# Performance work log

Measured on AMD Instinct MI355X. Metric: run time of the kernel, lower is better.

Reference implementation:

```python
import jax, jax.numpy as jnp
import numpy as np

PC = (-60.0, -60.0, -4.0, 140.0, 60.0, 4.0)
BEV_H, BEV_W, E, HEADS, LVLS, PTS, ZN, CAMS = 50, 50, 256, 8, 3, 4, 4, 6
HD = E // HEADS
IMG_H, IMG_W = 512.0, 800.0
SHAPES = ((64, 100), (32, 50), (16, 25))
FFN = 2 * E
EPS = 1e-5


def grid_sample(img, grid):
    # img (B,C,H,W), grid (B,Hg,Wg,2) in [-1,1]; bilinear, zeros padding, align_corners=False
    B, C, H, W = img.shape
    Hg, Wg = grid.shape[1], grid.shape[2]
    x = (grid[..., 0] + 1.0) * (W * 0.5) - 0.5
    y = (grid[..., 1] + 1.0) * (H * 0.5) - 0.5
    x0 = jnp.floor(x)
    y0 = jnp.floor(y)
    wx = x - x0
    wy = y - y0
    x0i = x0.astype(jnp.int32)
    y0i = y0.astype(jnp.int32)
    imgf = img.reshape(B, C, H * W)

    def gather(ix, iy):
        valid = ((ix >= 0) & (ix < W) & (iy >= 0) & (iy < H)).astype(img.dtype)
        idx = jnp.clip(iy, 0, H - 1) * W + jnp.clip(ix, 0, W - 1)
        idx = jnp.broadcast_to(idx.reshape(B, 1, Hg * Wg), (B, C, Hg * Wg))
        return jnp.take_along_axis(imgf, idx, axis=2).reshape(B, C, Hg, Wg) * valid[:, None]

    v00 = gather(x0i, y0i)
    v01 = gather(x0i + 1, y0i)
    v10 = gather(x0i, y0i + 1)
    v11 = gather(x0i + 1, y0i + 1)
    wx = wx[:, None]
    wy = wy[:, None]
    return v00 * (1 - wy) * (1 - wx) + v01 * (1 - wy) * wx + v10 * wy * (1 - wx) + v11 * wy * wx


def layer_norm(x, g, b):
    m = x.mean(-1, keepdims=True)
    v = ((x - m) ** 2).mean(-1, keepdims=True)
    return (x - m) / jnp.sqrt(v + 1e-5) * g + b


def get_reference_points():
    xs = (jnp.arange(BEV_W, dtype=jnp.float32) + 0.5) / BEV_W
    ys = (jnp.arange(BEV_H, dtype=jnp.float32) + 0.5) / BEV_H
    zs = (jnp.arange(ZN, dtype=jnp.float32) + 0.5) / ZN
    ref_y, ref_x = jnp.meshgrid(ys, xs, indexing='ij')
    xy = jnp.stack([ref_x, ref_y], -1).reshape(-1, 2)  # (HW,2)
    xy = jnp.broadcast_to(xy[:, None, :], (BEV_H * BEV_W, ZN, 2))
    z = jnp.broadcast_to(zs[None, :, None], (BEV_H * BEV_W, ZN, 1))
    r = jnp.concatenate([xy, z], -1)  # (HW,Z,3), normalized
    scale = jnp.array([PC[3] - PC[0], PC[4] - PC[1], PC[5] - PC[2]], jnp.float32)
    off = jnp.array([PC[0], PC[1], PC[2]], jnp.float32)
    return (r * scale + off).reshape(-1, 3)  # (HW*Z, 3)


def point_sampling(ref3d, l2i):
    # ref3d (Nq,3), l2i (B,N,4,4) -> ref2d (B,N,Nq,2), mask (B,N,Nq)
    Nq = ref3d.shape[0]
    pts = jnp.concatenate([ref3d, jnp.ones((Nq, 1), ref3d.dtype)], -1)
    cam = jnp.einsum('bnij,qj->bnqi', l2i, pts)
    d = cam[..., 2]
    u = cam[..., 0] / (d + EPS) / IMG_W
    v = cam[..., 1] / (d + EPS) / IMG_H
    ref2d = jnp.stack([u, v], -1)
    mask = (d > EPS) & (u > 0.0) & (u < 1.0) & (v > 0.0) & (v < 1.0)
    return ref2d, mask


def mha(q, k, v, fl):
    B = q.shape[0]
    wq, wk, wv = jnp.split(fl['ta_in_w'], 3, 0)
    bq, bk, bv = jnp.split(fl['ta_in_b'], 3, 0)
    Q = (q @ wq.T + bq).reshape(B, -1, HEADS, HD)
    K = (k @ wk.T + bk).reshape(B, -1, HEADS, HD)
    V = (v @ wv.T + bv).reshape(B, -1, HEADS, HD)
    a = jax.nn.softmax(jnp.einsum('bqhd,bkhd->bhqk', Q, K) / np.float32(np.sqrt(HD)), -1)
    o = jnp.einsum('bhqk,bkhd->bqhd', a, V).reshape(B, -1, E)
    return o @ fl['ta_out_w'].T + fl['ta_out_b']


def msda(query, qpos, value, ref, fl):
    # MultiScaleDeformableAttention (identity = zeros). ref (B,Nq,L,2) in [0,1].
    B, Nq, _ = query.shape
    q = query + qpos
    v = (value @ fl['vp_w'].T + fl['vp_b']).reshape(B, -1, HEADS, HD)
    off = (q @ fl['so_w'].T + fl['so_b']).reshape(B, Nq, HEADS, LVLS, PTS, 2)
    aw = jax.nn.softmax((q @ fl['aw_w'].T + fl['aw_b']).reshape(B, Nq, HEADS, LVLS * PTS), -1)
    aw = aw.reshape(B, Nq, HEADS, LVLS, PTS)
    norm = jnp.array([[w, h] for (h, w) in SHAPES], jnp.float32)  # (L,2) = (W,H)
    loc = ref[:, :, None, :, None, :] + off / norm[None, None, None, :, None, :]
    outs = []
    start = 0
    for l, (Hl, Wl) in enumerate(SHAPES):
        vl = v[:, start:start + Hl * Wl].transpose(0, 2, 3, 1).reshape(B * HEADS, HD, Hl, Wl)
        g = (2.0 * loc[:, :, :, l] - 1.0).transpose(0, 2, 1, 3, 4).reshape(B * HEADS, Nq, PTS, 2)
        outs.append(grid_sample(vl, g))  # (B*HEADS, HD, Nq, PTS)
        start += Hl * Wl
    s = jnp.stack(outs, 3)  # (B*HEADS, HD, Nq, L, P)
    w = aw.transpose(0, 2, 1, 3, 4).reshape(B * HEADS, 1, Nq, LVLS, PTS)
    o = (s * w).sum((3, 4)).reshape(B, HEADS, HD, Nq).transpose(0, 3, 1, 2).reshape(B, Nq, E)
    return o @ fl['op_w'].T + fl['op_b']


def spatial_attn(query, qpos, feats_t, l2i, ref3d, fl):
    B, Nq, _ = query.shape
    ref2d, mask = point_sampling(ref3d, l2i)
    out = jnp.zeros_like(query)
    valid = jnp.zeros((B, Nq), query.dtype)
    for cam in range(CAMS):
        value = jnp.concatenate(
            [f[:, cam].reshape(B, E, -1).transpose(0, 2, 1) for f in feats_t], axis=1)
        ref = jnp.broadcast_to(ref2d[:, cam][:, :, None, :], (B, Nq, LVLS, 2))
        a = msda(query, qpos, value, ref, fl)
        wgt = mask[:, cam].astype(query.dtype)
        out = out + a * wgt[..., None]
        valid = valid + wgt
    return out / jnp.maximum(valid, 1.0)[..., None]


def temporal_align(prev_bev, motion):
    B, C, H, W = prev_bev.shape
    xs = jnp.arange(W, dtype=prev_bev.dtype)
    ys = jnp.arange(H, dtype=prev_bev.dtype)
    yy, xx = jnp.meshgrid(ys, xs, indexing='ij')
    rx = (xx + 0.5) / W * (PC[3] - PC[0]) + PC[0]
    ry = (yy + 0.5) / H * (PC[4] - PC[1]) + PC[1]
    g = jnp.stack([rx, ry, jnp.zeros_like(rx), jnp.ones_like(rx)], -1)  # (H,W,4)
    inv = jnp.linalg.inv(motion)  # (B,4,4)
    gp = jnp.einsum('bij,hwj->bhwi', inv, g)
    nx = (gp[..., 0] - PC[0]) / (PC[3] - PC[0]) * 2.0 - 1.0
    ny = (gp[..., 1] - PC[1]) / (PC[4] - PC[1]) * 2.0 - 1.0
    return grid_sample(prev_bev, jnp.stack([nx, ny], -1))


def layer_fwd(bev, bev_pos, prev, feats_t, l2i, ref3d, fl):
    if prev is not None:
        attn = mha(bev + bev_pos, prev + bev_pos, prev, fl)
        bev = layer_norm(bev + attn, fl['n1_g'], fl['n1_b'])
    B, Nq, C = bev.shape
    bev_z = jnp.broadcast_to(bev[:, :, None, :], (B, Nq, ZN, C)).reshape(B, -1, C)
    pos_z = jnp.broadcast_to(bev_pos[:, :, None, :], (B, Nq, ZN, C)).reshape(B, -1, C)
    so = spatial_attn(bev_z, pos_z, feats_t, l2i, ref3d, fl)
    so = so.reshape(B, Nq, ZN, C).mean(2)
    bev = layer_norm(bev + so, fl['n2_g'], fl['n2_b'])
    h = jax.nn.relu(bev @ fl['ffn_w1'].T + fl['ffn_b1'])
    ffn = h @ fl['ffn_w2'].T + fl['ffn_b2']
    return layer_norm(bev + ffn, fl['n3_g'], fl['n3_b'])


def forward(fl, batch_size, seq_len):
    feats = [fl['feat0'], fl['feat1'], fl['feat2']]
    feats = [f.reshape(batch_size, seq_len, CAMS, E, f.shape[-2], f.shape[-1]) for f in feats]
    bev = jnp.broadcast_to(fl['bev_emb'][None], (batch_size, BEV_H * BEV_W, E))
    bev_pos = jnp.broadcast_to(fl['bev_pos_emb'][None], (batch_size, BEV_H * BEV_W, E))
    ref3d = get_reference_points()
    prev = None
    for t in range(seq_len):
        feats_t = [f[:, t] for f in feats]
        prev_al = None
        if prev is not None:
            pa = temporal_align(prev, fl['ego_motion'][:, t])
            prev_al = pa.reshape(batch_size, E, -1).transpose(0, 2, 1)
        bev_t = layer_fwd(bev, bev_pos, prev_al, feats_t, fl['lidar2img'][:, t], ref3d, fl)
        prev = bev_t.transpose(0, 2, 1).reshape(batch_size, E, BEV_H, BEV_W)
    return prev


def _make_cam_matrices():
    mats = np.zeros((CAMS, 4, 4), np.float32)
    K = np.array([[500.0, 0.0, 400.0], [0.0, 500.0, 256.0], [0.0, 0.0, 1.0]], np.float32)
    for i in range(CAMS):
        th = 2.0 * np.pi * i / CAMS
        xr = np.array([-np.sin(th), np.cos(th), 0.0])
        yr = np.array([0.0, 0.0, -1.0])
        fr = np.array([np.cos(th), np.sin(th), 0.0])
        R = np.stack([xr, yr, fr]).astype(np.float32)
        mats[i, :3, :3] = K @ R
        mats[i, 3, 3] = 1.0
    return mats


def setup_inputs() -> dict:
    key = jax.random.key(0)
    ks = jax.random.split(key, 20)
    rn = lambda k, s, sc=0.02: jax.random.normal(k, s, jnp.float32) * sc
    NOFF = HEADS * LVLS * PTS * 2
    NAW = HEADS * LVLS * PTS
    d = {
        'bev_emb': rn(ks[0], (BEV_H * BEV_W, E), 1.0),
        'bev_pos_emb': rn(ks[1], (BEV_H * BEV_W, E), 1.0),
        'ta_in_w': rn(ks[2], (3 * E, E)), 'ta_in_b': jnp.zeros(3 * E, jnp.float32),
        'ta_out_w': rn(ks[3], (E, E)), 'ta_out_b': jnp.zeros(E, jnp.float32),
        'so_w': rn(ks[4], (NOFF, E)), 'so_b': rn(ks[5], (NOFF,), 0.5),
        'aw_w': rn(ks[6], (NAW, E)), 'aw_b': jnp.zeros(NAW, jnp.float32),
        'vp_w': rn(ks[7], (E, E)), 'vp_b': jnp.zeros(E, jnp.float32),
        'op_w': rn(ks[8], (E, E)), 'op_b': jnp.zeros(E, jnp.float32),
        'ffn_w1': rn(ks[9], (FFN, E)), 'ffn_b1': jnp.zeros(FFN, jnp.float32),
        'ffn_w2': rn(ks[10], (E, FFN)), 'ffn_b2': jnp.zeros(E, jnp.float32),
        'n1_g': jnp.ones(E, jnp.float32), 'n1_b': jnp.zeros(E, jnp.float32),
        'n2_g': jnp.ones(E, jnp.float32), 'n2_b': jnp.zeros(E, jnp.float32),
        'n3_g': jnp.ones(E, jnp.float32), 'n3_b': jnp.zeros(E, jnp.float32),
        'feat0': rn(ks[11], (12, E, 64, 100), 1.0),
        'feat1': rn(ks[12], (12, E, 32, 50), 1.0),
        'feat2': rn(ks[13], (12, E, 16, 25), 1.0),
    }
    mats = _make_cam_matrices()  # realistic lidar->img projections per camera
    d['lidar2img'] = jnp.asarray(np.broadcast_to(mats, (1, 2, CAMS, 4, 4)).copy())
    em = np.tile(np.eye(4, dtype=np.float32), (1, 2, 1, 1))
    em[..., 0, 3] = 2.0  # 2m forward ego translation per step
    d['ego_motion'] = jnp.asarray(em)
    d['batch_size'] = 1
    d['seq_len'] = 2
    return d


def reference(bev_emb, bev_pos_emb, ta_in_w, ta_in_b, ta_out_w, ta_out_b,
              so_w, so_b, aw_w, aw_b, vp_w, vp_b, op_w, op_b,
              ffn_w1, ffn_b1, ffn_w2, ffn_b2,
              n1_g, n1_b, n2_g, n2_b, n3_g, n3_b,
              feat0, feat1, feat2, lidar2img, ego_motion, batch_size, seq_len):
    fl = dict(bev_emb=bev_emb, bev_pos_emb=bev_pos_emb, ta_in_w=ta_in_w, ta_in_b=ta_in_b,
              ta_out_w=ta_out_w, ta_out_b=ta_out_b, so_w=so_w, so_b=so_b, aw_w=aw_w, aw_b=aw_b,
              vp_w=vp_w, vp_b=vp_b, op_w=op_w, op_b=op_b, ffn_w1=ffn_w1, ffn_b1=ffn_b1,
              ffn_w2=ffn_w2, ffn_b2=ffn_b2, n1_g=n1_g, n1_b=n1_b, n2_g=n2_g, n2_b=n2_b,
              n3_g=n3_g, n3_b=n3_b, feat0=feat0, feat1=feat1, feat2=feat2,
              lidar2img=lidar2img, ego_motion=ego_motion)
    return forward(fl, int(batch_size), int(seq_len))
```

## Files before the change

### kernel.cpp

```cpp
#include <hip/hip_runtime.h>
#include <hip/hip_bf16.h>

#define NPIX   2500
#define EDIM   256
#define NHEADS 8
#define HDIM   32
#define NLVLS  3
#define NPTS   4
#define NZ     4
#define NCAMS  6
#define NQTOT  10000
#define NVAL   8400
#define FFND   512
#define NCHUNK 10
#define KVCH   250
#define VTROW  2504

typedef __attribute__((ext_vector_type(8))) short short8;
typedef __attribute__((ext_vector_type(4))) float float4v;

__device__ __forceinline__ void level_params(int l, int& H, int& W, int& st) {
    if (l == 0)      { H = 64; W = 100; st = 0;    }
    else if (l == 1) { H = 32; W = 50;  st = 6400; }
    else             { H = 16; W = 25;  st = 8000; }
}

__device__ __forceinline__ unsigned short f2bf(float x) {
    unsigned int u = __builtin_bit_cast(unsigned int, x);
    return (unsigned short)((u + 0x7fffu + ((u >> 16) & 1u)) >> 16);
}

__global__ __launch_bounds__(256) void transpose_feat_all_k(const float* __restrict__ feat0,
                                                            const float* __restrict__ feat1,
                                                            const float* __restrict__ feat2,
                                                            int t,
                                                            unsigned short* __restrict__ featT)
{
    const int cam = blockIdx.z;
    const int bx = blockIdx.x;
    const float* feat; int HW, lvl_off, p0;
    if (bx < 200)      { feat = feat0; HW = 6400; lvl_off = 0;    p0 = bx * 32;         }
    else if (bx < 250) { feat = feat1; HW = 1600; lvl_off = 6400; p0 = (bx - 200) * 32; }
    else               { feat = feat2; HW = 400;  lvl_off = 8000; p0 = (bx - 250) * 32; }
    const float* F = feat + (size_t)(t * NCAMS + cam) * EDIM * HW;
    unsigned short* T = featT + (size_t)cam * NVAL * EDIM;
    __shared__ float tile[32][33];
    const int e0 = blockIdx.y * 32;
    const int tp = threadIdx.x & 31, tr = threadIdx.x >> 5;
#pragma unroll
    for (int i = 0; i < 4; i++) {
        int e = e0 + tr + i * 8;
        int p = p0 + tp;
        tile[tr + i * 8][tp] = (p < HW) ? F[(size_t)e * HW + p] : 0.f;
    }
    __syncthreads();
#pragma unroll
    for (int i = 0; i < 4; i++) {
        int p = p0 + tr + i * 8;
        int e = e0 + tp;
        if (p < HW) T[(size_t)(lvl_off + p) * EDIM + e] = f2bf(tile[tp][tr + i * 8]);
    }
}

template<int ACT, int ADD>
__global__ __launch_bounds__(256) void gemm64_k(const float* __restrict__ A,
                                                const float* __restrict__ A2,
                                                const float* __restrict__ W,
                                                const float* __restrict__ bias,
                                                float* __restrict__ C,
                                                int M, int N, int K,
                                                size_t a_bs, size_t w_bs,
                                                size_t b_bs, size_t c_bs)
{
    __shared__ unsigned short As[64][44];
    __shared__ unsigned short Ws[64][44];
    const int m0 = blockIdx.y * 64;
    const int n0 = blockIdx.x * 64;
    const int tid = threadIdx.x;
    const float* Af = A + blockIdx.z * a_bs;
    const float* Wf = W + blockIdx.z * w_bs;
    const float* Bf = bias ? bias + blockIdx.z * b_bs : nullptr;
    float* Cb = C + blockIdx.z * c_bs;
    const int wave = tid >> 6, lane = tid & 63;
    const int wr = wave >> 1, wc = wave & 1;
    const int fr = lane & 15, fk = lane >> 4;
    float4v acc[2][2];
#pragma unroll
    for (int mi = 0; mi < 2; mi++)
#pragma unroll
        for (int ni = 0; ni < 2; ni++) { acc[mi][ni][0] = 0.f; acc[mi][ni][1] = 0.f;
                                         acc[mi][ni][2] = 0.f; acc[mi][ni][3] = 0.f; }
    const int srow = tid >> 2, sk = (tid & 3) * 8;
    for (int k0 = 0; k0 < K; k0 += 32) {
        unsigned short tmp[8];
        {
            const int gr = m0 + srow;
            if (gr < M) {
                const float* src = Af + (size_t)gr * K + k0 + sk;
                if (ADD) {
                    const float* src2 = A2 + (size_t)gr * K + k0 + sk;
#pragma unroll
                    for (int j = 0; j < 8; j++) tmp[j] = f2bf(src[j] + src2[j]);
                } else {
#pragma unroll
                    for (int j = 0; j < 8; j++) tmp[j] = f2bf(src[j]);
                }
            } else {
#pragma unroll
                for (int j = 0; j < 8; j++) tmp[j] = 0;
            }
            *(short8*)&As[srow][sk] = *(short8*)&tmp[0];
        }
        {
            const int gw = n0 + srow;
            if (gw < N) {
                const float* src = Wf + (size_t)gw * K + k0 + sk;
#pragma unroll
                for (int j = 0; j < 8; j++) tmp[j] = f2bf(src[j]);
            } else {
#pragma unroll
                for (int j = 0; j < 8; j++) tmp[j] = 0;
            }
            *(short8*)&Ws[srow][sk] = *(short8*)&tmp[0];
        }
        __syncthreads();
        short8 af[2], bfr[2];
#pragma unroll
        for (int mi = 0; mi < 2; mi++)
            af[mi] = *(const short8*)&As[wr * 32 + mi * 16 + fr][fk * 8];
#pragma unroll
        for (int ni = 0; ni < 2; ni++)
            bfr[ni] = *(const short8*)&Ws[wc * 32 + ni * 16 + fr][fk * 8];
#pragma unroll
        for (int mi = 0; mi < 2; mi++)
#pragma unroll
            for (int ni = 0; ni < 2; ni++)
                acc[mi][ni] = __builtin_amdgcn_mfma_f32_16x16x32_bf16(
                    af[mi], bfr[ni], acc[mi][ni], 0, 0, 0);
        __syncthreads();
    }
#pragma unroll
    for (int mi = 0; mi < 2; mi++)
#pragma unroll
        for (int ni = 0; ni < 2; ni++) {
            const int col = n0 + wc * 32 + ni * 16 + fr;
#pragma unroll
            for (int r = 0; r < 4; r++) {
                const int row = m0 + wr * 32 + mi * 16 + fk * 4 + r;
                if (row < M && col < N) {
                    float v = acc[mi][ni][r] + (Bf ? Bf[col] : 0.f);
                    if (ACT) v = fmaxf(v, 0.f);
                    Cb[(size_t)row * N + col] = v;
                }
            }
        }
}

template<int ACT, int ADD>
__global__ __launch_bounds__(256) void gemm64o_k(const float* __restrict__ A,
                                                 const float* __restrict__ A2,
                                                 const float* __restrict__ W,
                                                 const float* __restrict__ bias,
                                                 unsigned short* __restrict__ C,
                                                 int M, int N, int K)
{
    __shared__ unsigned short As[64][44];
    __shared__ unsigned short Ws[64][44];
    const int m0 = blockIdx.y * 64;
    const int n0 = blockIdx.x * 64;
    const int tid = threadIdx.x;
    const int wave = tid >> 6, lane = tid & 63;
    const int wr = wave >> 1, wc = wave & 1;
    const int fr = lane & 15, fk = lane >> 4;
    float4v acc[2][2];
#pragma unroll
    for (int mi = 0; mi < 2; mi++)
#pragma unroll
        for (int ni = 0; ni < 2; ni++) { acc[mi][ni][0] = 0.f; acc[mi][ni][1] = 0.f;
                                         acc[mi][ni][2] = 0.f; acc[mi][ni][3] = 0.f; }
    const int srow = tid >> 2, sk = (tid & 3) * 8;
    for (int k0 = 0; k0 < K; k0 += 32) {
        unsigned short tmp[8];
// ... 196 lines not shown
                for (int j = 0; j < 8; j++) tmp[j] = f2bf(src[j]);
            } else {
#pragma unroll
                for (int j = 0; j < 8; j++) tmp[j] = 0;
            }
            *(short8*)&Ws[srow][sk] = *(short8*)&tmp[0];
        }
        __syncthreads();
        short8 af[2], bfr[2];
#pragma unroll
        for (int mi = 0; mi < 2; mi++)
            af[mi] = *(const short8*)&As[wr * 32 + mi * 16 + fr][fk * 8];
#pragma unroll
        for (int ni = 0; ni < 2; ni++)
            bfr[ni] = *(const short8*)&Ws[wc * 32 + ni * 16 + fr][fk * 8];
#pragma unroll
        for (int mi = 0; mi < 2; mi++)
#pragma unroll
            for (int ni = 0; ni < 2; ni++)
                acc[mi][ni] = __builtin_amdgcn_mfma_f32_16x16x32_bf16(
                    af[mi], bfr[ni], acc[mi][ni], 0, 0, 0);
        __syncthreads();
    }
#pragma unroll
    for (int mi = 0; mi < 2; mi++)
#pragma unroll
        for (int ni = 0; ni < 2; ni++) {
            const int col = n0 + wc * 32 + ni * 16 + fr;
#pragma unroll
            for (int r = 0; r < 4; r++) {
                const int row = m0 + wr * 32 + mi * 16 + fk * 4 + r;
                if (row < M && col < N)
                    Cb[(size_t)row * N + col] = acc[mi][ni][r] + (bias ? bias[col] : 0.f);
            }
        }
}

__global__ __launch_bounds__(256) void gemm_vs_k(const unsigned short* __restrict__ featT,
                                                 const float* __restrict__ vp_w,
                                                 const float* __restrict__ vp_b,
                                                 float* __restrict__ vproj,
                                                 const float* __restrict__ Aso,
                                                 const float* __restrict__ A2so,
                                                 const float* __restrict__ Wso,
                                                 const float* __restrict__ Waw,
                                                 const float* __restrict__ Bso,
                                                 const float* __restrict__ Baw,
                                                 float* __restrict__ Cso)
{
    const int z = blockIdx.z;
    const bool so = (z == 6);
    if (!so && blockIdx.x >= 4) return;
    if (so && blockIdx.y >= 40) return;
    __shared__ unsigned short As[64][44];
    __shared__ unsigned short Ws[64][44];
    const int m0 = blockIdx.y * 64;
    const int n0 = blockIdx.x * 64;
    const int tid = threadIdx.x;
    const int wave = tid >> 6, lane = tid & 63;
    const int wr = wave >> 1, wc = wave & 1;
    const int fr = lane & 15, fk = lane >> 4;
    const unsigned short* Af = featT + (size_t)z * NVAL * EDIM;
    const int M = so ? NPIX : NVAL;
    float4v acc[2][2];
#pragma unroll
    for (int mi = 0; mi < 2; mi++)
#pragma unroll
        for (int ni = 0; ni < 2; ni++) { acc[mi][ni][0] = 0.f; acc[mi][ni][1] = 0.f;
                                         acc[mi][ni][2] = 0.f; acc[mi][ni][3] = 0.f; }
    const int srow = tid >> 2, sk = (tid & 3) * 8;
    for (int k0 = 0; k0 < EDIM; k0 += 32) {
        unsigned short tmp[8];
        {
            const int gr = m0 + srow;
            if (so) {
                if (gr < NPIX) {
                    const float* src  = Aso  + (size_t)gr * EDIM + k0 + sk;
                    const float* src2 = A2so + (size_t)gr * EDIM + k0 + sk;
#pragma unroll
                    for (int j = 0; j < 8; j++) tmp[j] = f2bf(src[j] + src2[j]);
                } else {
#pragma unroll
                    for (int j = 0; j < 8; j++) tmp[j] = 0;
                }
                *(short8*)&As[srow][sk] = *(short8*)&tmp[0];
            } else {
                if (gr < NVAL) {
                    *(short8*)&As[srow][sk] =
                        *(const short8*)&Af[(size_t)gr * EDIM + k0 + sk];
                } else {
                    short8 zr = {0,0,0,0,0,0,0,0};
                    *(short8*)&As[srow][sk] = zr;
                }
            }
        }
        {
            const int gw = n0 + srow;
            const float* src;
            if (so)
                src = (gw < 192) ? Wso + (size_t)gw * EDIM + k0 + sk
                    : (gw < 288) ? Waw + (size_t)(gw - 192) * EDIM + k0 + sk
                                 : nullptr;
            else
                src = vp_w + (size_t)gw * EDIM + k0 + sk;
            if (src) {
#pragma unroll
                for (int j = 0; j < 8; j++) tmp[j] = f2bf(src[j]);
            } else {
#pragma unroll
                for (int j = 0; j < 8; j++) tmp[j] = 0;
            }
            *(short8*)&Ws[srow][sk] = *(short8*)&tmp[0];
        }
        __syncthreads();
        short8 af[2], bfr[2];
#pragma unroll
        for (int mi = 0; mi < 2; mi++)
            af[mi] = *(const short8*)&As[wr * 32 + mi * 16 + fr][fk * 8];
#pragma unroll
        for (int ni = 0; ni < 2; ni++)
            bfr[ni] = *(const short8*)&Ws[wc * 32 + ni * 16 + fr][fk * 8];
#pragma unroll
        for (int mi = 0; mi < 2; mi++)
#pragma unroll
            for (int ni = 0; ni < 2; ni++)
                acc[mi][ni] = __builtin_amdgcn_mfma_f32_16x16x32_bf16(
                    af[mi], bfr[ni], acc[mi][ni], 0, 0, 0);
        __syncthreads();
    }
#pragma unroll
    for (int mi = 0; mi < 2; mi++)
#pragma unroll
        for (int ni = 0; ni < 2; ni++) {
            const int col = n0 + wc * 32 + ni * 16 + fr;
#pragma unroll
            for (int r = 0; r < 4; r++) {
                const int row = m0 + wr * 32 + mi * 16 + fk * 4 + r;
                if (row < M) {
                    if (so) {
                        if (col < 288) {
                            const float b = (col < 192) ? Bso[col] : Baw[col - 192];
                            Cso[(size_t)row * 288 + col] = acc[mi][ni][r] + b;
                        }
                    } else {
                        vproj[((size_t)z * NVAL + row) * EDIM + col] =
                            acc[mi][ni][r] + vp_b[col];
                    }
                }
            }
        }
}

__global__ __launch_bounds__(256) void gemm_op_k(const float* __restrict__ S,
                                                 const float* __restrict__ validn,
                                                 const float* __restrict__ W,
                                                 float* __restrict__ C)
{
    __shared__ unsigned short As[64][44];
    __shared__ unsigned short Ws[64][44];
    __shared__ float sfac[256];
    const int m0 = blockIdx.y * 64;
    const int n0 = blockIdx.x * 64;
    const int tid = threadIdx.x;
    {
        const int idx = m0 * 4 + tid;
        const float vn = (idx < NQTOT) ? validn[idx] : 1.f;
        sfac[tid] = 1.f / fmaxf(vn, 1.f);
    }
    __syncthreads();
    const int wave = tid >> 6, lane = tid & 63;
    const int wr = wave >> 1, wc = wave & 1;
    const int fr = lane & 15, fk = lane >> 4;
    float4v acc[2][2];
#pragma unroll
    for (int mi = 0; mi < 2; mi++)
#pragma unroll
        for (int ni = 0; ni < 2; ni++) { acc[mi][ni][0] = 0.f; acc[mi][ni][1] = 0.f;
                                         acc[mi][ni][2] = 0.f; acc[mi][ni][3] = 0.f; }
    const int srow = tid >> 2, sk = (tid & 3) * 8;
    for (int k0 = 0; k0 < EDIM; k0 += 32) {
        unsigned short tmp[8];
        {
            const int gr = m0 + srow;
            if (gr < NPIX) {
                float sum[8];
#pragma unroll
                for (int j = 0; j < 8; j++) sum[j] = 0.f;
#pragma unroll
                for (int iz = 0; iz < NZ; iz++) {
                    const float* src = S + ((size_t)(gr * 4 + iz) * EDIM + k0 + sk);
                    const float f = sfac[srow * 4 + iz];
#pragma unroll
                    for (int j = 0; j < 8; j++) sum[j] += src[j] * f;
                }
#pragma unroll
                for (int j = 0; j < 8; j++) tmp[j] = f2bf(sum[j] * 0.25f);
            } else {
#pragma unroll
                for (int j = 0; j < 8; j++) tmp[j] = 0;
            }
            *(short8*)&As[srow][sk] = *(short8*)&tmp[0];
        }
        {
            const float* src = W + (size_t)(n0 + srow) * EDIM + k0 + sk;
#pragma unroll
            for (int j = 0; j < 8; j++) tmp[j] = f2bf(src[j]);
            *(short8*)&Ws[srow][sk] = *(short8*)&tmp[0];
        }
        __syncthreads();
        short8 af[2], bfr[2];
#pragma unroll
        for (int mi = 0; mi < 2; mi++)
            af[mi] = *(const short8*)&As[wr * 32 + mi * 16 + fr][fk * 8];
#pragma unroll
        for (int ni = 0; ni < 2; ni++)
            bfr[ni] = *(const short8*)&Ws[wc * 32 + ni * 16 + fr][fk * 8];
#pragma unroll
        for (int mi = 0; mi < 2; mi++)
#pragma unroll
            for (int ni = 0; ni < 2; ni++)
                acc[mi][ni] = __builtin_amdgcn_mfma_f32_16x16x32_bf16(
                    af[mi], bfr[ni], acc[mi][ni], 0, 0, 0);
        __syncthreads();
    }
#pragma unroll
    for (int mi = 0; mi < 2; mi++)
#pragma unroll
        for (int ni = 0; ni < 2; ni++) {
            const int col = n0 + wc * 32 + ni * 16 + fr;
#pragma unroll
            for (int r = 0; r < 4; r++) {
                const int row = m0 + wr * 32 + mi * 16 + fk * 4 + r;
                if (row < NPIX)
                    C[(size_t)row * EDIM + col] = acc[mi][ni][r];
            }
        }
}

template<int TRANS>
__global__ __launch_bounds__(256) void resid_ln_k(const float* __restrict__ x0,
                                                  const float* __restrict__ x1,
                                                  const float* __restrict__ cvec,
                                                  const float* __restrict__ cscale,
                                                  const float* __restrict__ g,
                                                  const float* __restrict__ bta,
                                                  float* __restrict__ out)
{
    const int row = blockIdx.x, e = threadIdx.x;
    float x = x0[(size_t)row * EDIM + e] + x1[(size_t)row * EDIM + e];
    if (cvec) x += cvec[e] * cscale[row];
    __shared__ float red[256];
    red[e] = x; __syncthreads();
    for (int s = 128; s > 0; s >>= 1) { if (e < s) red[e] += red[e + s]; __syncthreads(); }
    float mean = red[0] * (1.f / 256.f);
    __syncthreads();
    float dx = x - mean;
    red[e] = dx * dx; __syncthreads();
    for (int s = 128; s > 0; s >>= 1) { if (e < s) red[e] += red[e + s]; __syncthreads(); }
    float var = red[0] * (1.f / 256.f);
    const float res = dx * rsqrtf(var + 1e-5f) * g[e] + bta[e];
    if (TRANS)
        out[(size_t)e * NPIX + row] = res;
    else
        out[(size_t)row * EDIM + e] = res;
}

__global__ void uv_aw_k(const float* __restrict__ l2i, int t,
                        const float* __restrict__ raw,
                        float* __restrict__ uvtab,
                        float* __restrict__ validn,
                        float* __restrict__ aw_soft,
                        float* __restrict__ vbm)
{
    if (blockIdx.x < 40) {
        const int n = blockIdx.x * 256 + threadIdx.x;
        if (n >= NQTOT) return;
        const int pix = n >> 2, iz = n & 3;
        const int prow = pix / 50, pcol = pix % 50;
        const float x3 = (pcol + 0.5f) * 4.0f - 60.f;
        const float y3 = (prow + 0.5f) * 2.4f - 60.f;
        const float z3 = (iz + 0.5f) * 2.0f - 4.f;
        int vcount = 0;
        float buf[12];
#pragma unroll
        for (int cam = 0; cam < NCAMS; cam++) {
            const float* Mt = l2i + (size_t)(t * NCAMS + cam) * 16;
            const float p0 = Mt[0] * x3 + Mt[1] * y3 + Mt[2]  * z3 + Mt[3];
            const float p1 = Mt[4] * x3 + Mt[5] * y3 + Mt[6]  * z3 + Mt[7];
            const float p2 = Mt[8] * x3 + Mt[9] * y3 + Mt[10] * z3 + Mt[11];
            const float dd = p2 + 1e-5f;
            const float u = p0 / dd * (1.f / 800.f);
            const float v = p1 / dd * (1.f / 512.f);
            const bool valid = (p2 > 1e-5f) && (u > 0.f) && (u < 1.f) &&
                               (v > 0.f) && (v < 1.f);
            if (valid) vcount++;
            buf[cam * 2]     = valid ? u : -1.f;
            buf[cam * 2 + 1] = v;
        }
#pragma unroll
        for (int j = 0; j < 12; j++) uvtab[(size_t)n * 12 + j] = buf[j];
        validn[n] = (float)vcount;
        float ind = (vcount > 0) ? 1.f : 0.f;
        ind += __shfl_xor(ind, 1);
        ind += __shfl_xor(ind, 2);
        if (iz == 0) vbm[pix] = ind * 0.25f;
    } else {
        const int gidx = (blockIdx.x - 40) * 256 + threadIdx.x;
        if (gidx >= NPIX * NHEADS) return;
        const int pix = gidx / NHEADS, h = gidx % NHEADS;
        const float* p = raw + (size_t)pix * 288 + 192 + h * 12;
        float m = -3.0e38f;
#pragma unroll
        for (int j = 0; j < 12; j++) m = fmaxf(m, p[j]);
        float e[12]; float s = 0.f;
#pragma unroll
        for (int j = 0; j < 12; j++) { e[j] = __expf(p[j] - m); s += e[j]; }
        const float inv = 1.f / s;
        float* o = aw_soft + (size_t)pix * 96 + h * 12;
#pragma unroll
        for (int j = 0; j < 12; j++) o[j] = e[j] * inv;
    }
}

__global__ __launch_bounds__(256) void spatial_sample_k(const float* __restrict__ vproj,
                                                        const float* __restrict__ offb,
                                                        const float* __restrict__ awb,
                                                        const float* __restrict__ uvtab,
                                                        float* __restrict__ S)
{
    const int n = blockIdx.x;
    const int tid = threadIdx.x;
    const int wave = tid >> 6, lane = tid & 63;
    const int ch0 = lane << 2;
    const int h = lane >> 3;
    const int pix = n >> 2;
    __shared__ float soff[192];
    __shared__ float saw[96];
    __shared__ float suv[12];
    __shared__ float red[3][256];
    if (tid < 192) soff[tid] = offb[(size_t)pix * 288 + tid];
    if (tid < 96)  saw[tid]  = awb[(size_t)pix * 96 + tid];
    if (tid >= 192 && tid < 204) suv[tid - 192] = uvtab[(size_t)n * 12 + (tid - 192)];
    __syncthreads();
    float4 acc = make_float4(0.f, 0.f, 0.f, 0.f);
    for (int cam = 0; cam < NCAMS; cam++) {
        const float u = suv[cam * 2];
        if (u < 0.f) continue;
        const float v = suv[cam * 2 + 1];
        const float* vc = vproj + (size_t)cam * NVAL * EDIM + ch0;
        for (int pt = wave; pt < NLVLS * NPTS; pt += 4) {
            const int l = pt >> 2, p = pt & 3;
            int Hl, Wl, st; level_params(l, Hl, Wl, st);
            const int ob = ((h * NLVLS + l) * NPTS + p) * 2;
            const float x = u * (float)Wl + soff[ob]     - 0.5f;
            const float y = v * (float)Hl + soff[ob + 1] - 0.5f;
            const float xf = floorf(x), yf = floorf(y);
            const float wx = x - xf, wy = y - yf;
            const int x0 = (int)xf, y0 = (int)yf;
            const float a = saw[(h * NLVLS + l) * NPTS + p];
            const bool xi0 = (x0 >= 0) & (x0 < Wl);
            const bool xi1 = (x0 + 1 >= 0) & (x0 + 1 < Wl);
            const bool yi0 = (y0 >= 0) & (y0 < Hl);
            const bool yi1 = (y0 + 1 >= 0) & (y0 + 1 < Hl);
            const int rb = st + y0 * Wl + x0;
            float4 sv = make_float4(0.f, 0.f, 0.f, 0.f);
            if (yi0 & xi0) {
                const float w00 = (1.f - wy) * (1.f - wx);
                const float4 t4 = *(const float4*)(vc + ((size_t)rb << 8));
                sv.x += w00 * t4.x; sv.y += w00 * t4.y; sv.z += w00 * t4.z; sv.w += w00 * t4.w;
            }
            if (yi0 & xi1) {
                const float w01 = (1.f - wy) * wx;
                const float4 t4 = *(const float4*)(vc + ((size_t)(rb + 1) << 8));
                sv.x += w01 * t4.x; sv.y += w01 * t4.y; sv.z += w01 * t4.z; sv.w += w01 * t4.w;
            }
            if (yi1 & xi0) {
                const float w10 = wy * (1.f - wx);
                const float4 t4 = *(const float4*)(vc + ((size_t)(rb + Wl) << 8));
                sv.x += w10 * t4.x; sv.y += w10 * t4.y; sv.z += w10 * t4.z; sv.w += w10 * t4.w;
            }
            if (yi1 & xi1) {
                const float w11 = wy * wx;
                const float4 t4 = *(const float4*)(vc + ((size_t)(rb + Wl + 1) << 8));
                sv.x += w11 * t4.x; sv.y += w11 * t4.y; sv.z += w11 * t4.z; sv.w += w11 * t4.w;
            }
            acc.x += a * sv.x; acc.y += a * sv.y; acc.z += a * sv.z; acc.w += a * sv.w;
        }
    }
    if (wave > 0) *(float4*)&red[wave - 1][ch0] = acc;
    __syncthreads();
    if (wave == 0) {
#pragma unroll
        for (int w2 = 0; w2 < 3; w2++) {
            const float4 r4 = *(const float4*)&red[w2][ch0];
            acc.x += r4.x; acc.y += r4.y; acc.z += r4.z; acc.w += r4.w;
        }
        *(float4*)(S + (size_t)n * EDIM + ch0) = acc;
    }
}

__global__ __launch_bounds__(256) void talign_k(const float* __restrict__ prev,
                                                const float* __restrict__ motion,
                                                float* __restrict__ out)
{
    __shared__ float sinv[16];
    if (threadIdx.x == 0) {
        float a[4][8];
        for (int i = 0; i < 4; i++)
            for (int j = 0; j < 4; j++) { a[i][j] = motion[i * 4 + j];
                                          a[i][4 + j] = (i == j) ? 1.f : 0.f; }
        for (int col = 0; col < 4; col++) {
            int piv = col;
            for (int r = col + 1; r < 4; r++)
                if (fabsf(a[r][col]) > fabsf(a[piv][col])) piv = r;
            if (piv != col)
                for (int j = 0; j < 8; j++) { float tp = a[col][j];
                                              a[col][j] = a[piv][j]; a[piv][j] = tp; }
            float idv = 1.f / a[col][col];
            for (int j = 0; j < 8; j++) a[col][j] *= idv;
            for (int r = 0; r < 4; r++) {
                if (r == col) continue;
                float f = a[r][col];
                for (int j = 0; j < 8; j++) a[r][j] -= f * a[col][j];
            }
        }
        for (int i = 0; i < 4; i++)
            for (int j = 0; j < 4; j++) sinv[i * 4 + j] = a[i][4 + j];
    }
    __syncthreads();
    const int pix = blockIdx.x, e = threadIdx.x;
    const int r = pix / 50, c = pix % 50;
    const float rx = (c + 0.5f) * 4.0f - 60.f;
    const float ry = (r + 0.5f) * 2.4f - 60.f;
    const float gx = sinv[0] * rx + sinv[1] * ry + sinv[3];
    const float gy = sinv[4] * rx + sinv[5] * ry + sinv[7];
    const float nx = (gx + 60.f) * 0.01f - 1.f;
    const float ny = (gy + 60.f) * (1.f / 60.f) - 1.f;
    const float x = (nx + 1.f) * 25.f - 0.5f;
    const float y = (ny + 1.f) * 25.f - 0.5f;
    const float xf = floorf(x), yf = floorf(y);
    const float wx = x - xf, wy = y - yf;
    const int x0 = (int)xf, y0 = (int)yf;
    bool xi0 = (x0 >= 0 && x0 < 50), xi1 = (x0 + 1 >= 0 && x0 + 1 < 50);
    bool yi0 = (y0 >= 0 && y0 < 50), yi1 = (y0 + 1 >= 0 && y0 + 1 < 50);
    float s = 0.f;
    if (yi0 && xi0) s += (1.f - wy) * (1.f - wx) * prev[(size_t)(y0 * 50 + x0) * EDIM + e];
    if (yi0 && xi1) s += (1.f - wy) * wx         * prev[(size_t)(y0 * 50 + x0 + 1) * EDIM + e];
    if (yi1 && xi0) s += wy * (1.f - wx)         * prev[(size_t)((y0 + 1) * 50 + x0) * EDIM + e];
    if (yi1 && xi1) s += wy * wx                 * prev[(size_t)((y0 + 1) * 50 + x0 + 1) * EDIM + e];
    out[(size_t)pix * EDIM + e] = s;
}

__global__ __launch_bounds__(256) void mha_mfma_k(const unsigned short* __restrict__ Qbf,
                                                  const unsigned short* __restrict__ Kbf,
                                                  const unsigned short* __restrict__ VbfT,
                                                  float* __restrict__ pacc,
                                                  float* __restrict__ pml)
{
    const int h = blockIdx.y;
    const int q0 = blockIdx.x * 64;
    const int chunk = blockIdx.z;
    const int kv0 = chunk * KVCH;
    const int kv1 = min(NPIX, kv0 + KVCH);
    const int tid = threadIdx.x;
    const int wave = tid >> 6, lane = tid & 63;
    const int fr = lane & 15, fk = lane >> 4;

    __shared__ unsigned short Qs[64][44];
    __shared__ unsigned short Ks[64][44];
    __shared__ unsigned short Vt[32][76];
    __shared__ unsigned short Ps[4][16][76];

    const int srow = tid >> 2, scs = tid & 3;
    {
        const int gq = q0 + srow;
        if (gq < NPIX)
            *(short8*)&Qs[srow][scs * 8] =
                *(const short8*)&Qbf[(size_t)gq * EDIM + h * HDIM + scs * 8];
        else {
            short8 z = {0,0,0,0,0,0,0,0};
            *(short8*)&Qs[srow][scs * 8] = z;
        }
    }
    __syncthreads();
    const short8 aq = *(const short8*)&Qs[wave * 16 + fr][fk * 8];

    float m[4], l[4];
    float4v o0, o1;
#pragma unroll
    for (int r = 0; r < 4; r++) { m[r] = -3.0e38f; l[r] = 0.f; o0[r] = 0.f; o1[r] = 0.f; }

    const int vd = tid >> 3, vpart = tid & 7;
    for (int kb = kv0; kb < kv1; kb += 64) {
        __syncthreads();
        {
// ... 8 lines not shown
            const unsigned short* vrow = VbfT + (size_t)(h * HDIM + vd) * VTROW;
            const int base = kb + vpart * 8;
            if (base + 8 <= kv1) {
                *(short8*)&Vt[vd][vpart * 8] = *(const short8*)&vrow[base];
            } else {
#pragma unroll
                for (int j = 0; j < 8; j++)
                    Vt[vd][vpart * 8 + j] = (base + j < kv1) ? vrow[base + j] : 0;
            }
        }
        __syncthreads();
        float4v s[4];
#pragma unroll
        for (int t = 0; t < 4; t++) {
            const short8 bk = *(const short8*)&Ks[t * 16 + fr][fk * 8];
            float4v z; z[0] = 0.f; z[1] = 0.f; z[2] = 0.f; z[3] = 0.f;
            s[t] = __builtin_amdgcn_mfma_f32_16x16x32_bf16(aq, bk, z, 0, 0, 0);
        }
        if (kb + 64 > kv1) {
#pragma unroll
            for (int t = 0; t < 4; t++) {
                const int colg = kb + t * 16 + fr;
                if (colg >= kv1) { s[t][0] = -3.0e38f; s[t][1] = -3.0e38f;
                                   s[t][2] = -3.0e38f; s[t][3] = -3.0e38f; }
            }
        }
        float cand[4];
#pragma unroll
        for (int r = 0; r < 4; r++)
            cand[r] = fmaxf(fmaxf(s[0][r], s[1][r]), fmaxf(s[2][r], s[3][r]));
#pragma unroll
        for (int off = 1; off < 16; off <<= 1)
#pragma unroll
            for (int r = 0; r < 4; r++)
                cand[r] = fmaxf(cand[r], __shfl_xor(cand[r], off));
        float corr[4];
#pragma unroll
        for (int r = 0; r < 4; r++) {
            const float mn = fmaxf(m[r], cand[r]);
            corr[r] = __expf(m[r] - mn);
            m[r] = mn;
        }
        float psum[4];
#pragma unroll
        for (int r = 0; r < 4; r++) psum[r] = 0.f;
#pragma unroll
        for (int t = 0; t < 4; t++)
#pragma unroll
            for (int r = 0; r < 4; r++) {
                const float p = __expf(s[t][r] - m[r]);
                psum[r] += p;
                Ps[wave][fk * 4 + r][t * 16 + fr] = f2bf(p);
            }
#pragma unroll
        for (int off = 1; off < 16; off <<= 1)
#pragma unroll
            for (int r = 0; r < 4; r++)
                psum[r] += __shfl_xor(psum[r], off);
#pragma unroll
        for (int r = 0; r < 4; r++) {
            l[r] = l[r] * corr[r] + psum[r];
            o0[r] *= corr[r];
            o1[r] *= corr[r];
        }
        const short8 ap0 = *(const short8*)&Ps[wave][fr][fk * 8];
        const short8 ap1 = *(const short8*)&Ps[wave][fr][32 + fk * 8];
        {
            const short8 bv0 = *(const short8*)&Vt[fr][fk * 8];
            const short8 bv1 = *(const short8*)&Vt[fr][32 + fk * 8];
            o0 = __builtin_amdgcn_mfma_f32_16x16x32_bf16(ap0, bv0, o0, 0, 0, 0);
            o0 = __builtin_amdgcn_mfma_f32_16x16x32_bf16(ap1, bv1, o0, 0, 0, 0);
        }
        {
            const short8 bv0 = *(const short8*)&Vt[16 + fr][fk * 8];
            const short8 bv1 = *(const short8*)&Vt[16 + fr][32 + fk * 8];
            o1 = __builtin_amdgcn_mfma_f32_16x16x32_bf16(ap0, bv0, o1, 0, 0, 0);
            o1 = __builtin_amdgcn_mfma_f32_16x16x32_bf16(ap1, bv1, o1, 0, 0, 0);
        }
    }
#pragma unroll
    for (int r = 0; r < 4; r++) {
        const int q = q0 + wave * 16 + fk * 4 + r;
        if (q < NPIX) {
            const size_t pi = ((size_t)chunk * NPIX + q) * NHEADS + h;
            pacc[pi * 32 + fr]      = o0[r];
            pacc[pi * 32 + 16 + fr] = o1[r];
            if (fr == 0) { pml[pi * 2] = m[r]; pml[pi * 2 + 1] = l[r]; }
        }
    }
}

__global__ __launch_bounds__(256) void mha_merge_k(const float* __restrict__ pacc,
                                                   const float* __restrict__ pml,
                                                   unsigned short* __restrict__ O)
{
    const int q = blockIdx.x;
    const int tid = threadIdx.x;
    const int h = tid >> 5, d = tid & 31;
    float ms[NCHUNK], ls[NCHUNK];
    float gm = -3.0e38f;
#pragma unroll
    for (int c = 0; c < NCHUNK; c++) {
        const size_t pi = ((size_t)c * NPIX + q) * NHEADS + h;
        ms[c] = pml[pi * 2];
        ls[c] = pml[pi * 2 + 1];
        gm = fmaxf(gm, ms[c]);
    }
    float gl = 0.f, s = 0.f;
#pragma unroll
    for (int c = 0; c < NCHUNK; c++) {
        const size_t pi = ((size_t)c * NPIX + q) * NHEADS + h;
        float w = __expf(ms[c] - gm);
        gl += ls[c] * w;
        s  += pacc[pi * 32 + d] * w;
    }
    O[(size_t)q * EDIM + h * HDIM + d] = f2bf(s / gl);
}

extern "C" void kernel_launch(void* const* d_in, const int* in_sizes, int n_in,
                              void* d_out, int out_size, void* d_ws, size_t ws_size,
                              hipStream_t stream)
{
    const float* bev_emb  = (const float*)d_in[0];
    const float* bev_pose = (const float*)d_in[1];
    const float* ta_in_w  = (const float*)d_in[2];
    const float* ta_in_b  = (const float*)d_in[3];
    const float* ta_out_w = (const float*)d_in[4];
    const float* ta_out_b = (const float*)d_in[5];
    const float* so_w     = (const float*)d_in[6];
    const float* so_b     = (const float*)d_in[7];
    const float* aw_w     = (const float*)d_in[8];
    const float* aw_b     = (const float*)d_in[9];
    const float* vp_w     = (const float*)d_in[10];
    const float* vp_b     = (const float*)d_in[11];
    const float* op_w     = (const float*)d_in[12];
    const float* op_b     = (const float*)d_in[13];
    const float* ffn_w1   = (const float*)d_in[14];
    const float* ffn_b1   = (const float*)d_in[15];
    const float* ffn_w2   = (const float*)d_in[16];
    const float* ffn_b2   = (const float*)d_in[17];
    const float* n1_g     = (const float*)d_in[18];
    const float* n1_b     = (const float*)d_in[19];
    const float* n2_g     = (const float*)d_in[20];
    const float* n2_b     = (const float*)d_in[21];
    const float* n3_g     = (const float*)d_in[22];
    const float* n3_b     = (const float*)d_in[23];
    const float* feat0    = (const float*)d_in[24];
    const float* feat1    = (const float*)d_in[25];
    const float* feat2    = (const float*)d_in[26];
    const float* l2i      = (const float*)d_in[27];
    const float* ego      = (const float*)d_in[28];

    float* w = (float*)d_ws;
    float* ws_inv   = w;
    float* validn   = w + 16;
    float* vbm      = w + 10016;
    float* bev_cur  = w + 16384;
    float* bev_prev = bev_cur  + 640000;
    float* qin      = bev_prev + 640000;
    float* kin      = qin      + 640000;
    float* prev_al  = kin      + 640000;
    float* Qb       = prev_al  + 640000;
    float* Kb       = Qb       + 640000;
    float* Vb       = Kb       + 640000;
    float* attn_pre = Vb       + 640000;
    float* attn_o   = attn_pre + 640000;
    float* off_buf  = attn_o   + 640000;
    float* aw_raw   = off_buf  + 480000;
    float* aw_soft  = aw_raw   + 240000;
    float* Sm       = aw_soft  + 240000;
    float* vproj    = Sm       + 640000;
    float* Sbuf     = Qb;
    float* ffn_h    = kin;
    float* pacc     = vproj;
    float* pml      = vproj + (size_t)NCHUNK * NPIX * NHEADS * 32;
    unsigned short* featT = (unsigned short*)qin;
    float* uvtab = attn_o;
    unsigned short* Qbf  = (unsigned short*)attn_o;
    unsigned short* Kbf  = Qbf + 640000;
    unsigned short* VbfT = (unsigned short*)off_buf;
    unsigned short* attn_pre_bf = (unsigned short*)attn_pre;
    unsigned short* ffn_hbf = (unsigned short*)ffn_h;
    (void)aw_raw; (void)Qb; (void)Kb; (void)Vb; (void)ws_inv; (void)Sm;

    auto GEMM = [&](const float* A, const float* Wp, const float* bias, float* C,
                    int M, int N, int K, int act) {
        dim3 g((N + 63) / 64, (M + 63) / 64);
        if (act)
            gemm64_k<1, 0><<<g, 256, 0, stream>>>(A, nullptr, Wp, bias, C, M, N, K,
                                                  0, 0, 0, 0);
        else
            gemm64_k<0, 0><<<g, 256, 0, stream>>>(A, nullptr, Wp, bias, C, M, N, K,
                                                  0, 0, 0, 0);
    };

    for (int t = 0; t < 2; t++) {
        const float* cur = bev_emb;
        if (t > 0) {
            talign_k<<<NPIX, 256, 0, stream>>>(bev_prev, ego + (size_t)t * 16, prev_al);
            gemm_qkv_k<<<dim3(4, 40, 3), 256, 0, stream>>>(
                bev_emb, prev_al, bev_pose, ta_in_w, ta_in_b, Qbf, Kbf, VbfT);
            mha_mfma_k<<<dim3((NPIX + 63) / 64, NHEADS, NCHUNK), 256, 0, stream>>>(
                Qbf, Kbf, VbfT, pacc, pml);
            mha_merge_k<<<NPIX, 256, 0, stream>>>(pacc, pml, attn_pre_bf);
            gemm64b_k<<<dim3(4, 40), 256, 0, stream>>>(
                attn_pre_bf, ta_out_w, ta_out_b, attn_o, NPIX, EDIM, EDIM, 0, 0);
            resid_ln_k<0><<<NPIX, 256, 0, stream>>>(bev_emb, attn_o, nullptr, nullptr,
                                                    n1_g, n1_b, bev_cur);
            cur = bev_cur;
        }
        transpose_feat_all_k<<<dim3(263, 8, 6), 256, 0, stream>>>(
            feat0, feat1, feat2, t, featT);
        gemm_vs_k<<<dim3(5, 132, 7), 256, 0, stream>>>(
            featT, vp_w, vp_b, vproj, cur, bev_pose, so_w, aw_w, so_b, aw_b, off_buf);
        uv_aw_k<<<119, 256, 0, stream>>>(l2i, t, off_buf, uvtab, validn, aw_soft, vbm);
        spatial_sample_k<<<NQTOT, 256, 0, stream>>>(vproj, off_buf, aw_soft, uvtab, Sbuf);
        gemm_op_k<<<dim3(4, 40), 256, 0, stream>>>(Sbuf, validn, op_w, attn_o);
        resid_ln_k<0><<<NPIX, 256, 0, stream>>>(cur, attn_o, op_b, vbm,
                                                n2_g, n2_b, bev_cur);
        gemm64o_k<1, 0><<<dim3(8, 40), 256, 0, stream>>>(
            bev_cur, nullptr, ffn_w1, ffn_b1, ffn_hbf, NPIX, FFND, EDIM);
        gemm64b_k<<<dim3(4, 40), 256, 0, stream>>>(
            ffn_hbf, ffn_w2, ffn_b2, attn_o, NPIX, EDIM, FFND, 0, 0);
        if (t == 0)
            resid_ln_k<0><<<NPIX, 256, 0, stream>>>(bev_cur, attn_o, nullptr, nullptr,
                                                    n3_g, n3_b, bev_prev);
        else
            resid_ln_k<1><<<NPIX, 256, 0, stream>>>(bev_cur, attn_o, nullptr, nullptr,
                                                    n3_g, n3_b, (float*)d_out);
    }
}
```

Baseline: 390.2 us.

## Remove uv_aw kernel by recomputing projections and softmax in consumers

Drops the separate uv_aw_k launch. Camera projection, valid counts and the BEV mask are now recomputed inside spatial_sample_k, gemm_op_k and resid_ln_k, and the attention-weight softmax moves into spatial_sample_k, which reads the raw logits directly. This removes one launch per timestep and the global round trips for uvtab, validn, vbm and aw_soft. In exchange the projection and softmax math runs redundantly per block, and an extra __syncthreads is added in spatial sampling.

```diff
diff --git a/kernel.cpp b/kernel.cpp
--- a/kernel.cpp
+++ b/kernel.cpp
@@ -28,6 +28,22 @@
 __device__ __forceinline__ unsigned short f2bf(float x) {
     unsigned int u = __builtin_bit_cast(unsigned int, x);
     return (unsigned short)((u + 0x7fffu + ((u >> 16) & 1u)) >> 16);
+}
+
+__device__ __forceinline__ bool cam_project(const float* __restrict__ Mt,
+                                            int pix, int iz, float& u, float& v)
+{
+    const int prow = pix / 50, pcol = pix % 50;
+    const float x3 = (pcol + 0.5f) * 4.0f - 60.f;
+    const float y3 = (prow + 0.5f) * 2.4f - 60.f;
+    const float z3 = (iz + 0.5f) * 2.0f - 4.f;
+    const float p0 = Mt[0] * x3 + Mt[1] * y3 + Mt[2]  * z3 + Mt[3];
+    const float p1 = Mt[4] * x3 + Mt[5] * y3 + Mt[6]  * z3 + Mt[7];
+    const float p2 = Mt[8] * x3 + Mt[9] * y3 + Mt[10] * z3 + Mt[11];
+    const float dd = p2 + 1e-5f;
+    u = p0 / dd * (1.f / 800.f);
+    v = p1 / dd * (1.f / 512.f);
+    return (p2 > 1e-5f) && (u > 0.f) && (u < 1.f) && (v > 0.f) && (v < 1.f);
 }
 
 __global__ __launch_bounds__(256) void transpose_feat_all_k(const float* __restrict__ feat0,
@@ -530,7 +546,7 @@
 }
 
 __global__ __launch_bounds__(256) void gemm_op_k(const float* __restrict__ S,
-                                                 const float* __restrict__ validn,
+                                                 const float* __restrict__ l2i, int t,
                                                  const float* __restrict__ W,
                                                  float* __restrict__ C)
 {
@@ -542,8 +558,19 @@
     const int tid = threadIdx.x;
     {
         const int idx = m0 * 4 + tid;
-        const float vn = (idx < NQTOT) ? validn[idx] : 1.f;
-        sfac[tid] = 1.f / fmaxf(vn, 1.f);
+        float sf = 1.f;
+        if (idx < NQTOT) {
+            const int pix = idx >> 2, iz = idx & 3;
+            int vcount = 0;
+#pragma unroll
+            for (int cam = 0; cam < NCAMS; cam++) {
+                float u, v;
+                if (cam_project(l2i + (size_t)(t * NCAMS + cam) * 16, pix, iz, u, v))
+                    vcount++;
+            }
+            sf = 1.f / fmaxf((float)vcount, 1.f);
+        }
+        sfac[tid] = sf;
     }
     __syncthreads();
     const int wave = tid >> 6, lane = tid & 63;
@@ -615,19 +642,36 @@
         }
 }
 
-template<int TRANS>
+template<int TRANS, int VBM>
 __global__ __launch_bounds__(256) void resid_ln_k(const float* __restrict__ x0,
                                                   const float* __restrict__ x1,
                                                   const float* __restrict__ cvec,
-                                                  const float* __restrict__ cscale,
+                                                  const float* __restrict__ l2i, int t,
                                                   const float* __restrict__ g,
                                                   const float* __restrict__ bta,
                                                   float* __restrict__ out)
 {
     const int row = blockIdx.x, e = threadIdx.x;
+    __shared__ float red[256];
+    __shared__ float svbm;
+    if (VBM) {
+        if (e < 4) {
+            int vcount = 0;
+#pragma unroll
+            for (int cam = 0; cam < NCAMS; cam++) {
+                float u, v;
+                if (cam_project(l2i + (size_t)(t * NCAMS + cam) * 16, row, e, u, v))
+                    vcount++;
+            }
+            float ind = (vcount > 0) ? 1.f : 0.f;
+            ind += __shfl_xor(ind, 1);
+            ind += __shfl_xor(ind, 2);
+            if (e == 0) svbm = ind * 0.25f;
+        }
+        __syncthreads();
+    }
     float x = x0[(size_t)row * EDIM + e] + x1[(size_t)row * EDIM + e];
-    if (cvec) x += cvec[e] * cscale[row];
-    __shared__ float red[256];
+    if (VBM) x += cvec[e] * svbm;
     red[e] = x; __syncthreads();
     for (int s = 128; s > 0; s >>= 1) { if (e < s) red[e] += red[e + s]; __syncthreads(); }
     float mean = red[0] * (1.f / 256.f);
@@ -643,67 +687,10 @@
         out[(size_t)row * EDIM + e] = res;
 }
 
-__global__ void uv_aw_k(const float* __restrict__ l2i, int t,
-                        const float* __restrict__ raw,
-                        float* __restrict__ uvtab,
-                        float* __restrict__ validn,
-                        float* __restrict__ aw_soft,
-                        float* __restrict__ vbm)
-{
-    if (blockIdx.x < 40) {
-        const int n = blockIdx.x * 256 + threadIdx.x;
-        if (n >= NQTOT) return;
-        const int pix = n >> 2, iz = n & 3;
-        const int prow = pix / 50, pcol = pix % 50;
-        const float x3 = (pcol + 0.5f) * 4.0f - 60.f;
-        const float y3 = (prow + 0.5f) * 2.4f - 60.f;
-        const float z3 = (iz + 0.5f) * 2.0f - 4.f;
-        int vcount = 0;
-        float buf[12];
-#pragma unroll
-        for (int cam = 0; cam < NCAMS; cam++) {
-            const float* Mt = l2i + (size_t)(t * NCAMS + cam) * 16;
-            const float p0 = Mt[0] * x3 + Mt[1] * y3 + Mt[2]  * z3 + Mt[3];
-            const float p1 = Mt[4] * x3 + Mt[5] * y3 + Mt[6]  * z3 + Mt[7];
-            const float p2 = Mt[8] * x3 + Mt[9] * y3 + Mt[10] * z3 + Mt[11];
-            const float dd = p2 + 1e-5f;
-            const float u = p0 / dd * (1.f / 800.f);
-            const float v = p1 / dd * (1.f / 512.f);
-            const bool valid = (p2 > 1e-5f) && (u > 0.f) && (u < 1.f) &&
-                               (v > 0.f) && (v < 1.f);
-            if (valid) vcount++;
-            buf[cam * 2]     = valid ? u : -1.f;
-            buf[cam * 2 + 1] = v;
-        }
-#pragma unroll
-        for (int j = 0; j < 12; j++) uvtab[(size_t)n * 12 + j] = buf[j];
-        validn[n] = (float)vcount;
-        float ind = (vcount > 0) ? 1.f : 0.f;
-        ind += __shfl_xor(ind, 1);
-        ind += __shfl_xor(ind, 2);
-        if (iz == 0) vbm[pix] = ind * 0.25f;
-    } else {
-        const int gidx = (blockIdx.x - 40) * 256 + threadIdx.x;
-        if (gidx >= NPIX * NHEADS) return;
-        const int pix = gidx / NHEADS, h = gidx % NHEADS;
-        const float* p = raw + (size_t)pix * 288 + 192 + h * 12;
-        float m = -3.0e38f;
-#pragma unroll
-        for (int j = 0; j < 12; j++) m = fmaxf(m, p[j]);
-        float e[12]; float s = 0.f;
-#pragma unroll
-        for (int j = 0; j < 12; j++) { e[j] = __expf(p[j] - m); s += e[j]; }
-        const float inv = 1.f / s;
-        float* o = aw_soft + (size_t)pix * 96 + h * 12;
-#pragma unroll
-        for (int j = 0; j < 12; j++) o[j] = e[j] * inv;
-    }
-}
-
 __global__ __launch_bounds__(256) void spatial_sample_k(const float* __restrict__ vproj,
                                                         const float* __restrict__ offb,
-                                                        const float* __restrict__ awb,
-                                                        const float* __restrict__ uvtab,
+                                                        const float* __restrict__ l2i,
+                                                        int t,
                                                         float* __restrict__ S)
 {
     const int n = blockIdx.x;
@@ -717,8 +704,26 @@
     __shared__ float suv[12];
     __shared__ float red[3][256];
     if (tid < 192) soff[tid] = offb[(size_t)pix * 288 + tid];
-    if (tid < 96)  saw[tid]  = awb[(size_t)pix * 96 + tid];
-    if (tid >= 192 && tid < 204) suv[tid - 192] = uvtab[(size_t)n * 12 + (tid - 192)];
+    if (tid < 96)  saw[tid]  = offb[(size_t)pix * 288 + 192 + tid];
+    if (tid < 6) {
+        float u, v;
+        const bool valid = cam_project(l2i + (size_t)(t * NCAMS + tid) * 16,
+                                       pix, n & 3, u, v);
+        suv[tid * 2]     = valid ? u : -1.f;
+        suv[tid * 2 + 1] = v;
+    }
+    __syncthreads();
+    if (tid < 8) {
+        float m = -3.0e38f;
+#pragma unroll
+        for (int j = 0; j < 12; j++) m = fmaxf(m, saw[tid * 12 + j]);
+        float ex[12]; float s = 0.f;
+#pragma unroll
+        for (int j = 0; j < 12; j++) { ex[j] = __expf(saw[tid * 12 + j] - m); s += ex[j]; }
+        const float inv = 1.f / s;
+#pragma unroll
+        for (int j = 0; j < 12; j++) saw[tid * 12 + j] = ex[j] * inv;
+    }
     __syncthreads();
     float4 acc = make_float4(0.f, 0.f, 0.f, 0.f);
     for (int cam = 0; cam < NCAMS; cam++) {
@@ -1033,9 +1038,6 @@
     const float* ego      = (const float*)d_in[28];
 
     float* w = (float*)d_ws;
-    float* ws_inv   = w;
-    float* validn   = w + 16;
-    float* vbm      = w + 10016;
     float* bev_cur  = w + 16384;
     float* bev_prev = bev_cur  + 640000;
     float* qin      = bev_prev + 640000;
@@ -1056,13 +1058,12 @@
     float* pacc     = vproj;
     float* pml      = vproj + (size_t)NCHUNK * NPIX * NHEADS * 32;
     unsigned short* featT = (unsigned short*)qin;
-    float* uvtab = attn_o;
     unsigned short* Qbf  = (unsigned short*)attn_o;
     unsigned short* Kbf  = Qbf + 640000;
     unsigned short* VbfT = (unsigned short*)off_buf;
     unsigned short* attn_pre_bf = (unsigned short*)attn_pre;
     unsigned short* ffn_hbf = (unsigned short*)ffn_h;
-    (void)aw_raw; (void)Qb; (void)Kb; (void)Vb; (void)ws_inv; (void)Sm;
+    (void)aw_raw; (void)aw_soft; (void)Sm; (void)Qb; (void)Kb; (void)Vb;
 
     auto GEMM = [&](const float* A, const float* Wp, const float* bias, float* C,
                     int M, int N, int K, int act) {
@@ -1086,28 +1087,27 @@
             mha_merge_k<<<NPIX, 256, 0, stream>>>(pacc, pml, attn_pre_bf);
             gemm64b_k<<<dim3(4, 40), 256, 0, stream>>>(
                 attn_pre_bf, ta_out_w, ta_out_b, attn_o, NPIX, EDIM, EDIM, 0, 0);
-            resid_ln_k<0><<<NPIX, 256, 0, stream>>>(bev_emb, attn_o, nullptr, nullptr,
-                                                    n1_g, n1_b, bev_cur);
+            resid_ln_k<0, 0><<<NPIX, 256, 0, stream>>>(
+                bev_emb, attn_o, nullptr, nullptr, 0, n1_g, n1_b, bev_cur);
             cur = bev_cur;
         }
         transpose_feat_all_k<<<dim3(263, 8, 6), 256, 0, stream>>>(
             feat0, feat1, feat2, t, featT);
         gemm_vs_k<<<dim3(5, 132, 7), 256, 0, stream>>>(
             featT, vp_w, vp_b, vproj, cur, bev_pose, so_w, aw_w, so_b, aw_b, off_buf);
-        uv_aw_k<<<119, 256, 0, stream>>>(l2i, t, off_buf, uvtab, validn, aw_soft, vbm);
-        spatial_sample_k<<<NQTOT, 256, 0, stream>>>(vproj, off_buf, aw_soft, uvtab, Sbuf);
-        gemm_op_k<<<dim3(4, 40), 256, 0, stream>>>(Sbuf, validn, op_w, attn_o);
-        resid_ln_k<0><<<NPIX, 256, 0, stream>>>(cur, attn_o, op_b, vbm,
-                                                n2_g, n2_b, bev_cur);
+        spatial_sample_k<<<NQTOT, 256, 0, stream>>>(vproj, off_buf, l2i, t, Sbuf);
+        gemm_op_k<<<dim3(4, 40), 256, 0, stream>>>(Sbuf, l2i, t, op_w, attn_o);
+        resid_ln_k<0, 1><<<NPIX, 256, 0, stream>>>(
+            cur, attn_o, op_b, l2i, t, n2_g, n2_b, bev_cur);
         gemm64o_k<1, 0><<<dim3(8, 40), 256, 0, stream>>>(
             bev_cur, nullptr, ffn_w1, ffn_b1, ffn_hbf, NPIX, FFND, EDIM);
         gemm64b_k<<<dim3(4, 40), 256, 0, stream>>>(
             ffn_hbf, ffn_w2, ffn_b2, attn_o, NPIX, EDIM, FFND, 0, 0);
         if (t == 0)
-            resid_ln_k<0><<<NPIX, 256, 0, stream>>>(bev_cur, attn_o, nullptr, nullptr,
-                                                    n3_g, n3_b, bev_prev);
+            resid_ln_k<0, 0><<<NPIX, 256, 0, stream>>>(
+                bev_cur, attn_o, nullptr, nullptr, 0, n3_g, n3_b, bev_prev);
         else
-            resid_ln_k<1><<<NPIX, 256, 0, stream>>>(bev_cur, attn_o, nullptr, nullptr,
-                                                    n3_g, n3_b, (float*)d_out);
-    }
-}
+            resid_ln_k<1, 0><<<NPIX, 256, 0, stream>>>(
+                bev_cur, attn_o, nullptr, nullptr, 0, n3_g, n3_b, (float*)d_out);
+    }
+}
```

Measured after the change: 398.8 us. +2.2%, slower.
